# Performance work log

Measured on AMD Instinct MI355X. Metric: run time of the kernel, lower is better.

Reference implementation:

```python
import jax, jax.numpy as jnp
import numpy as np

N = 8192   # nodes
F = 128    # features
ORDER = 4  # polynomial taps


def setup_inputs() -> dict:
    key = jax.random.key(0)
    k1, k2, k3 = jax.random.split(key, 3)
    X = jax.random.normal(k1, (N, F), dtype=jnp.float32)
    # scale GSO so powers don't blow up (spectral-norm-ish normalization)
    S = jax.random.normal(k2, (N, N), dtype=jnp.float32) / jnp.sqrt(jnp.float32(N))
    coefficients = jax.random.uniform(k3, (ORDER,), dtype=jnp.float32)
    return {"X": X, "S": S, "coefficients": coefficients}


def reference(X, S, coefficients):
    # y = sum_{k=0}^{K-1} h_k * S^k X
    Z = X
    y = coefficients[0] * Z
    for k in range(1, ORDER):  # small fixed tap count; loop over taps, not data
        Z = S @ Z              # S^k X, [N, F]
        y = y + coefficients[k] * Z
    return y
```

## Files before the change

kernel.cpp:

```cpp
#include <hip/hip_runtime.h>
#include <hip/hip_bf16.h>
#include <stdint.h>


typedef __attribute__((ext_vector_type(8))) short     bf16x8;
typedef __attribute__((ext_vector_type(8))) uint16_t  u16x8;
typedef __attribute__((ext_vector_type(4))) float     f32x4;

#define NN 8192
#define NF 128
#define ZSTRIDE (8192 + 64)

#define WAITV(n) asm volatile("s_waitcnt vmcnt(" #n ")" ::: "memory")
#define WAITL0   asm volatile("s_waitcnt lgkmcnt(0)" ::: "memory")

__device__ inline uint16_t f2bf(float f) {
    uint32_t u = __builtin_bit_cast(uint32_t, f);
    u += 0x7fffu + ((u >> 16) & 1u);
    return (uint16_t)(u >> 16);
}

__device__ inline void gl2lds16(const void* g, uint8_t* l) {
    __builtin_amdgcn_global_load_lds(
        (const __attribute__((address_space(1))) uint32_t*)g,
        (__attribute__((address_space(3))) uint32_t*)l,
        16, 0, 0);
}

__device__ inline bf16x8 ld16(const uint8_t* p) {
    return __builtin_bit_cast(bf16x8, *(const u16x8*)p);
}

__global__ __launch_bounds__(256) void k_convert(const float* __restrict__ S,
                                                 uint16_t* __restrict__ S16) {
    const size_t n8 = (size_t)NN * NN / 8;
    const size_t stride = (size_t)gridDim.x * 256;
    for (size_t i = (size_t)blockIdx.x * 256 + threadIdx.x; i < n8; i += stride) {
        f32x4 a = __builtin_nontemporal_load((const f32x4*)(S + i * 8));
        f32x4 b = __builtin_nontemporal_load((const f32x4*)(S + i * 8 + 4));
        u16x8 p;
#pragma unroll
        for (int j = 0; j < 4; ++j) { p[j] = f2bf(a[j]); p[j + 4] = f2bf(b[j]); }
        *(u16x8*)(S16 + i * 8) = p;
    }
}

__global__ __launch_bounds__(256) void k_prep(const float* __restrict__ X,
                                              const float* __restrict__ coeff,
                                              float* __restrict__ y,
                                              uint16_t* __restrict__ ZT0) {
    __shared__ float tile[16][NF + 4];
    const int t  = threadIdx.x;
    const int r0 = blockIdx.x * 16;
    const float h0 = coeff[0];
#pragma unroll
    for (int i = 0; i < 2; ++i) {
        int o   = (i * 256 + t) * 4;
        int row = o >> 7, col = o & 127;
        f32x4 v = *(const f32x4*)(X + (size_t)(r0 + row) * NF + col);
        *(f32x4*)&tile[row][col] = v;
        *(f32x4*)(y + (size_t)(r0 + row) * NF + col) = v * h0;
    }
    __syncthreads();
    const int c = t >> 1, rh = t & 1;
    u16x8 pk;
#pragma unroll
    for (int e = 0; e < 8; ++e) pk[e] = f2bf(tile[rh * 8 + e][c]);
    *(u16x8*)(ZT0 + (size_t)c * ZSTRIDE + r0 + rh * 8) = pk;
}

template<int KS>
__global__ __launch_bounds__(512, 4) void k_gemm_bf(
    const uint16_t* __restrict__ S16, const uint16_t* __restrict__ ZTin,
    float* __restrict__ P)
{
    __shared__ __align__(16) uint8_t smem[3][24576];
    const int t = threadIdx.x, lane = t & 63;
    const int w = t >> 6, m = lane & 15, g = lane >> 4;
    const int rt = w & 3, ch = w >> 2;
    const int mt = blockIdx.x & 127, ks = blockIdx.x >> 7;
    const int r0 = mt * 64;
    const int kb = ks * (NN / KS);
    constexpr int NT = (NN / KS) / 64;

    const int srow = t >> 3, sc = t & 7;
    const int scs  = (sc ^ (srow & 7)) << 3;
    const uint16_t* asrc = S16  + (size_t)(r0 + srow) * NN + kb + scs;
    const uint16_t* bsrc = ZTin + (size_t)srow * ZSTRIDE   + kb + scs;

    const int sw   = m & 7;
    const int aoff = (rt * 16 + m) * 128 + ((g ^ sw) << 4);
    const int bof  = 8192 + (ch * 64 + m) * 128 + ((g ^ sw) << 4);

    f32x4 acc[4] = {};

    auto stage = [&](int buf, int kt) {
        const int ko = kt * 64;
        uint8_t* b = smem[buf];
        gl2lds16(asrc + ko, b + t * 16);
        gl2lds16(bsrc + ko, b + 8192 + t * 16);
        gl2lds16(bsrc + (size_t)64 * ZSTRIDE + ko, b + 16384 + t * 16);
    };

    stage(0, 0);
    stage(1, 1);
    int cur = 0;
#pragma unroll 1
    for (int kt = 0; kt < NT; ++kt) {
        if (kt + 2 < NT) {
            int nxt = cur + 2; if (nxt >= 3) nxt -= 3;
            stage(nxt, kt + 2);
            WAITV(6);
        } else if (kt + 2 == NT) {
            WAITV(3);
        } else {
            WAITV(0);
        }
        __builtin_amdgcn_s_barrier();
        __builtin_amdgcn_sched_barrier(0);
        const uint8_t* bb = smem[cur];
        bf16x8 a0 = ld16(bb + aoff);
        bf16x8 a1 = ld16(bb + (aoff ^ 64));
#pragma unroll
        for (int ct = 0; ct < 4; ++ct) {
            acc[ct] = __builtin_amdgcn_mfma_f32_16x16x32_bf16(
                a0, ld16(bb + bof + ct * 16 * 128), acc[ct], 0, 0, 0);
            acc[ct] = __builtin_amdgcn_mfma_f32_16x16x32_bf16(
                a1, ld16(bb + ((bof + ct * 16 * 128) ^ 64)), acc[ct], 0, 0, 0);
        }
        WAITL0;
        __builtin_amdgcn_sched_barrier(0);
        __builtin_amdgcn_s_barrier();
        cur = (cur + 1 == 3) ? 0 : cur + 1;
    }

    float* pb = P + ((size_t)ks * NN + r0 + rt * 16 + 4 * g) * NF + ch * 64 + m;
#pragma unroll
    for (int ct = 0; ct < 4; ++ct)
#pragma unroll
        for (int i = 0; i < 4; ++i)
            pb[(size_t)i * NF + ct * 16] = acc[ct][i];
}

template<int KS, bool WRITE_ZT>
__global__ __launch_bounds__(256) void k_combine(const float* __restrict__ P,
                                                 float* __restrict__ y,
                                                 uint16_t* __restrict__ ZTout,
                                                 const float* __restrict__ coeff,
                                                 int pass) {
    __shared__ float tile[16][NF + 4];
    const int t = threadIdx.x, r0 = blockIdx.x * 16;
    const float hk = coeff[pass];
    const int row = t >> 4, col = (t & 15) * 8;
    const size_t off = (size_t)(r0 + row) * NF + col;
    f32x4 s0 = *(const f32x4*)(P + off);
    f32x4 s1 = *(const f32x4*)(P + off + 4);
#pragma unroll
    for (int k = 1; k < KS; ++k) {
        s0 += *(const f32x4*)(P + (size_t)k * NN * NF + off);
        s1 += *(const f32x4*)(P + (size_t)k * NN * NF + off + 4);
    }
    float* yp = y + off;
    f32x4 y0 = *(const f32x4*)yp, y1 = *(const f32x4*)(yp + 4);
    *(f32x4*)yp       = y0 + hk * s0;
    *(f32x4*)(yp + 4) = y1 + hk * s1;
    if (WRITE_ZT) {
        *(f32x4*)&tile[row][col]     = s0;
        *(f32x4*)&tile[row][col + 4] = s1;
        __syncthreads();
        const int c = t >> 1, rh = t & 1;
        u16x8 pk;
#pragma unroll
        for (int e = 0; e < 8; ++e) pk[e] = f2bf(tile[rh * 8 + e][c]);
        *(u16x8*)(ZTout + (size_t)c * ZSTRIDE + r0 + rh * 8) = pk;
    }
}

template<int KS>
static void run(const float* X, const float* S, const float* coeff, float* y,
                uint16_t* ZT0, uint16_t* ZT1, uint16_t* S16, float* P,
                hipStream_t stream) {
    k_prep<<<dim3(512), dim3(256), 0, stream>>>(X, coeff, y, ZT0);
    k_convert<<<dim3(2048), dim3(256), 0, stream>>>(S, S16);
    k_gemm_bf<KS><<<dim3(128 * KS), dim3(512), 0, stream>>>(S16, ZT0, P);
    k_combine<KS, true ><<<dim3(512), dim3(256), 0, stream>>>(P, y, ZT1, coeff, 1);
    k_gemm_bf<KS><<<dim3(128 * KS), dim3(512), 0, stream>>>(S16, ZT1, P);
    k_combine<KS, true ><<<dim3(512), dim3(256), 0, stream>>>(P, y, ZT0, coeff, 2);
    k_gemm_bf<KS><<<dim3(128 * KS), dim3(512), 0, stream>>>(S16, ZT0, P);
    k_combine<KS, false><<<dim3(512), dim3(256), 0, stream>>>(P, y, nullptr, coeff, 3);
}

extern "C" void kernel_launch(void* const* d_in, const int* in_sizes, int n_in,
                              void* d_out, int out_size, void* d_ws, size_t ws_size,
                              hipStream_t stream) {
    const float* X     = (const float*)d_in[0];
    const float* S     = (const float*)d_in[1];
    const float* coeff = (const float*)d_in[2];
    float* y = (float*)d_out;

    uint8_t* ws = (uint8_t*)d_ws;
    const size_t zb     = ((size_t)NF * ZSTRIDE * sizeof(uint16_t) + 255) & ~(size_t)255;
    const size_t s16b   = (size_t)NN * NN * sizeof(uint16_t);
    const size_t base   = 2 * zb + s16b;
    const size_t pslice = (size_t)NN * NF * sizeof(float);
    uint16_t* ZT0 = (uint16_t*)ws;
    uint16_t* ZT1 = (uint16_t*)(ws + zb);
    uint16_t* S16 = (uint16_t*)(ws + 2 * zb);
    float*    P   = (float*)(ws + base);

    if (ws_size >= base + 4 * pslice)
        run<4>(X, S, coeff, y, ZT0, ZT1, S16, P, stream);
    else if (ws_size >= base + 2 * pslice)
        run<2>(X, S, coeff, y, ZT0, ZT1, S16, P, stream);
    else
        run<1>(X, S, coeff, y, ZT0, ZT1, S16, P, stream);
}
```

Before: 187.0 us.

## Fuse S fp32-to-bf16 conversion into first GEMM and use double buffering

Removes the standalone conversion kernel: each block of the first GEMM converts its own 64-row by K-slice stripe of S to bf16, writes it to the workspace, then runs the GEMM on that stripe, which it reads back from cache. This avoids a separate launch and lets the first GEMM's reads of S16 hit freshly written lines in L2. It also reduces the LDS pipeline from three buffers to two, lowering LDS use per block at the cost of shallower prefetch for all three GEMMs. Each block's conversion is serialized before its GEMM, so there is no overlap inside a block.

```diff
diff --git a/kernel.cpp b/kernel.cpp
--- a/kernel.cpp
+++ b/kernel.cpp
@@ -29,20 +29,6 @@
 
 __device__ inline bf16x8 ld16(const uint8_t* p) {
     return __builtin_bit_cast(bf16x8, *(const u16x8*)p);
-}
-
-__global__ __launch_bounds__(256) void k_convert(const float* __restrict__ S,
-                                                 uint16_t* __restrict__ S16) {
-    const size_t n8 = (size_t)NN * NN / 8;
-    const size_t stride = (size_t)gridDim.x * 256;
-    for (size_t i = (size_t)blockIdx.x * 256 + threadIdx.x; i < n8; i += stride) {
-        f32x4 a = __builtin_nontemporal_load((const f32x4*)(S + i * 8));
-        f32x4 b = __builtin_nontemporal_load((const f32x4*)(S + i * 8 + 4));
-        u16x8 p;
-#pragma unroll
-        for (int j = 0; j < 4; ++j) { p[j] = f2bf(a[j]); p[j + 4] = f2bf(b[j]); }
-        *(u16x8*)(S16 + i * 8) = p;
-    }
 }
 
 __global__ __launch_bounds__(256) void k_prep(const float* __restrict__ X,
@@ -69,56 +55,30 @@
     *(u16x8*)(ZT0 + (size_t)c * ZSTRIDE + r0 + rh * 8) = pk;
 }
 
-template<int KS>
-__global__ __launch_bounds__(512, 4) void k_gemm_bf(
-    const uint16_t* __restrict__ S16, const uint16_t* __restrict__ ZTin,
-    float* __restrict__ P)
-{
-    __shared__ __align__(16) uint8_t smem[3][24576];
-    const int t = threadIdx.x, lane = t & 63;
-    const int w = t >> 6, m = lane & 15, g = lane >> 4;
-    const int rt = w & 3, ch = w >> 2;
-    const int mt = blockIdx.x & 127, ks = blockIdx.x >> 7;
-    const int r0 = mt * 64;
-    const int kb = ks * (NN / KS);
-    constexpr int NT = (NN / KS) / 64;
-
-    const int srow = t >> 3, sc = t & 7;
-    const int scs  = (sc ^ (srow & 7)) << 3;
-    const uint16_t* asrc = S16  + (size_t)(r0 + srow) * NN + kb + scs;
-    const uint16_t* bsrc = ZTin + (size_t)srow * ZSTRIDE   + kb + scs;
-
-    const int sw   = m & 7;
-    const int aoff = (rt * 16 + m) * 128 + ((g ^ sw) << 4);
-    const int bof  = 8192 + (ch * 64 + m) * 128 + ((g ^ sw) << 4);
-
-    f32x4 acc[4] = {};
-
+template<int NT>
+__device__ inline void gemm_core(const uint16_t* asrc, const uint16_t* bsrc,
+                                 uint8_t* smem, int t, f32x4 (&acc)[4],
+                                 int aoff, int bof) {
     auto stage = [&](int buf, int kt) {
         const int ko = kt * 64;
-        uint8_t* b = smem[buf];
+        uint8_t* b = smem + buf * 24576;
         gl2lds16(asrc + ko, b + t * 16);
         gl2lds16(bsrc + ko, b + 8192 + t * 16);
         gl2lds16(bsrc + (size_t)64 * ZSTRIDE + ko, b + 16384 + t * 16);
     };
-
     stage(0, 0);
-    stage(1, 1);
     int cur = 0;
 #pragma unroll 1
     for (int kt = 0; kt < NT; ++kt) {
-        if (kt + 2 < NT) {
-            int nxt = cur + 2; if (nxt >= 3) nxt -= 3;
-            stage(nxt, kt + 2);
-            WAITV(6);
-        } else if (kt + 2 == NT) {
+        if (kt + 1 < NT) {
+            stage(cur ^ 1, kt + 1);
             WAITV(3);
         } else {
             WAITV(0);
         }
         __builtin_amdgcn_s_barrier();
         __builtin_amdgcn_sched_barrier(0);
-        const uint8_t* bb = smem[cur];
+        const uint8_t* bb = smem + cur * 24576;
         bf16x8 a0 = ld16(bb + aoff);
         bf16x8 a1 = ld16(bb + (aoff ^ 64));
 #pragma unroll
@@ -131,8 +91,88 @@
         WAITL0;
         __builtin_amdgcn_sched_barrier(0);
         __builtin_amdgcn_s_barrier();
-        cur = (cur + 1 == 3) ? 0 : cur + 1;
-    }
+        cur ^= 1;
+    }
+}
+
+template<int KS>
+__global__ __launch_bounds__(512, 4) void k_gemm_bf(
+    const uint16_t* __restrict__ S16, const uint16_t* __restrict__ ZTin,
+    float* __restrict__ P)
+{
+    __shared__ __align__(16) uint8_t smem[2][24576];
+    const int t = threadIdx.x, lane = t & 63;
+    const int w = t >> 6, m = lane & 15, g = lane >> 4;
+    const int rt = w & 3, ch = w >> 2;
+    const int mt = blockIdx.x & 127, ks = blockIdx.x >> 7;
+    const int r0 = mt * 64;
+    const int kb = ks * (NN / KS);
+    constexpr int NT = (NN / KS) / 64;
+
+    const int srow = t >> 3, sc = t & 7;
+    const int scs  = (sc ^ (srow & 7)) << 3;
+    const uint16_t* asrc = S16  + (size_t)(r0 + srow) * NN + kb + scs;
+    const uint16_t* bsrc = ZTin + (size_t)srow * ZSTRIDE   + kb + scs;
+
+    const int sw   = m & 7;
+    const int aoff = (rt * 16 + m) * 128 + ((g ^ sw) << 4);
+    const int bof  = 8192 + (ch * 64 + m) * 128 + ((g ^ sw) << 4);
+
+    f32x4 acc[4] = {};
+    gemm_core<NT>(asrc, bsrc, &smem[0][0], t, acc, aoff, bof);
+
+    float* pb = P + ((size_t)ks * NN + r0 + rt * 16 + 4 * g) * NF + ch * 64 + m;
+#pragma unroll
+    for (int ct = 0; ct < 4; ++ct)
+#pragma unroll
+        for (int i = 0; i < 4; ++i)
+            pb[(size_t)i * NF + ct * 16] = acc[ct][i];
+}
+
+template<int KS>
+__global__ __launch_bounds__(512, 4) void k_gemm_cv2(
+    const float* __restrict__ Sf, const uint16_t* __restrict__ S16,
+    const uint16_t* __restrict__ ZTin, float* __restrict__ P)
+{
+    __shared__ __align__(16) uint8_t smem[2][24576];
+    const int t = threadIdx.x, lane = t & 63;
+    const int w = t >> 6, m = lane & 15, g = lane >> 4;
+    const int rt = w & 3, ch = w >> 2;
+    const int mt = blockIdx.x & 127, ks = blockIdx.x >> 7;
+    const int r0 = mt * 64;
+    const int kb = ks * (NN / KS);
+    constexpr int KSL = NN / KS;
+    constexpr int NT  = KSL / 64;
+    constexpr int C8  = KSL / 8;
+    constexpr int ITERS = 64 * KSL / (512 * 8);
+
+    uint16_t* S16w = (uint16_t*)S16;
+#pragma unroll 4
+    for (int it = 0; it < ITERS; ++it) {
+        int id  = it * 512 + t;
+        int row = id / C8, c8 = id % C8;
+        size_t off = (size_t)(r0 + row) * NN + kb + c8 * 8;
+        f32x4 a = *(const f32x4*)(Sf + off);
+        f32x4 b = *(const f32x4*)(Sf + off + 4);
+        u16x8 p;
+#pragma unroll
+        for (int j = 0; j < 4; ++j) { p[j] = f2bf(a[j]); p[j + 4] = f2bf(b[j]); }
+        *(u16x8*)(S16w + off) = p;
+    }
+    WAITV(0);
+    __syncthreads();
+
+    const int srow = t >> 3, sc = t & 7;
+    const int scs  = (sc ^ (srow & 7)) << 3;
+    const uint16_t* asrc = S16  + (size_t)(r0 + srow) * NN + kb + scs;
+    const uint16_t* bsrc = ZTin + (size_t)srow * ZSTRIDE   + kb + scs;
+
+    const int sw   = m & 7;
+    const int aoff = (rt * 16 + m) * 128 + ((g ^ sw) << 4);
+    const int bof  = 8192 + (ch * 64 + m) * 128 + ((g ^ sw) << 4);
+
+    f32x4 acc[4] = {};
+    gemm_core<NT>(asrc, bsrc, &smem[0][0], t, acc, aoff, bof);
 
     float* pb = P + ((size_t)ks * NN + r0 + rt * 16 + 4 * g) * NF + ch * 64 + m;
 #pragma unroll
@@ -181,8 +221,7 @@
                 uint16_t* ZT0, uint16_t* ZT1, uint16_t* S16, float* P,
                 hipStream_t stream) {
     k_prep<<<dim3(512), dim3(256), 0, stream>>>(X, coeff, y, ZT0);
-    k_convert<<<dim3(2048), dim3(256), 0, stream>>>(S, S16);
-    k_gemm_bf<KS><<<dim3(128 * KS), dim3(512), 0, stream>>>(S16, ZT0, P);
+    k_gemm_cv2<KS><<<dim3(128 * KS), dim3(512), 0, stream>>>(S, S16, ZT0, P);
     k_combine<KS, true ><<<dim3(512), dim3(256), 0, stream>>>(P, y, ZT1, coeff, 1);
     k_gemm_bf<KS><<<dim3(128 * KS), dim3(512), 0, stream>>>(S16, ZT1, P);
     k_combine<KS, true ><<<dim3(512), dim3(256), 0, stream>>>(P, y, ZT0, coeff, 2);
```

Result: slower. 196.1 us (+4.8%).

## Pre-tile S into contiguous bf16 blocks per GEMM workgroup tile

Applied to the files above, without the earlier changes.

The fp32-to-bf16 conversion of S now writes it in a tiled layout, so each GEMM workgroup's A operand for every k-step is one contiguous 8 KB block instead of 64 strided row segments. This makes the global-to-LDS loads in the three GEMM passes fully sequential, aiming to improve DRAM/cache efficiency. The split-K factor is hardcoded to 4, so the fallback paths for smaller workspaces are gone. The conversion kernel now uses normal rather than nontemporal loads plus an LDS staging step.

```diff
diff --git a/kernel.cpp b/kernel.cpp
--- a/kernel.cpp
+++ b/kernel.cpp
@@ -29,20 +29,6 @@
 
 __device__ inline bf16x8 ld16(const uint8_t* p) {
     return __builtin_bit_cast(bf16x8, *(const u16x8*)p);
-}
-
-__global__ __launch_bounds__(256) void k_convert(const float* __restrict__ S,
-                                                 uint16_t* __restrict__ S16) {
-    const size_t n8 = (size_t)NN * NN / 8;
-    const size_t stride = (size_t)gridDim.x * 256;
-    for (size_t i = (size_t)blockIdx.x * 256 + threadIdx.x; i < n8; i += stride) {
-        f32x4 a = __builtin_nontemporal_load((const f32x4*)(S + i * 8));
-        f32x4 b = __builtin_nontemporal_load((const f32x4*)(S + i * 8 + 4));
-        u16x8 p;
-#pragma unroll
-        for (int j = 0; j < 4; ++j) { p[j] = f2bf(a[j]); p[j + 4] = f2bf(b[j]); }
-        *(u16x8*)(S16 + i * 8) = p;
-    }
 }
 
 __global__ __launch_bounds__(256) void k_prep(const float* __restrict__ X,
@@ -69,9 +55,41 @@
     *(u16x8*)(ZT0 + (size_t)c * ZSTRIDE + r0 + rh * 8) = pk;
 }
 
-template<int KS>
+__global__ __launch_bounds__(256) void k_convert_t(const float* __restrict__ S,
+                                                   uint16_t* __restrict__ S16T) {
+    __shared__ __align__(16) uint16_t lds[16384];
+    const int t = threadIdx.x, bx = blockIdx.x;
+    const int mt = bx & 127, ks = bx >> 7;
+    const int r0 = mt * 64, kb = ks * 2048;
+    uint16_t* tb = S16T + (size_t)(mt * 4 + ks) * 131072;
+
+#pragma unroll 1
+    for (int kc = 0; kc < 8; ++kc) {
+#pragma unroll
+        for (int si = 0; si < 8; ++si) {
+            int id = si * 256 + t;
+            int rr = id >> 5, c8 = id & 31;
+            const float* src = S + (size_t)(r0 + rr) * NN + kb + kc * 256 + c8 * 8;
+            f32x4 a = *(const f32x4*)src;
+            f32x4 b = *(const f32x4*)(src + 4);
+            u16x8 p;
+#pragma unroll
+            for (int j = 0; j < 4; ++j) { p[j] = f2bf(a[j]); p[j + 4] = f2bf(b[j]); }
+            *(u16x8*)&lds[((c8 >> 3) * 64 + rr) * 64 + (c8 & 7) * 8] = p;
+        }
+        __syncthreads();
+        uint16_t* dst = tb + kc * 16384;
+#pragma unroll
+        for (int si = 0; si < 8; ++si) {
+            int id = si * 256 + t;
+            *(u16x8*)(dst + id * 8) = *(const u16x8*)&lds[id * 8];
+        }
+        __syncthreads();
+    }
+}
+
 __global__ __launch_bounds__(512, 4) void k_gemm_bf(
-    const uint16_t* __restrict__ S16, const uint16_t* __restrict__ ZTin,
+    const uint16_t* __restrict__ S16T, const uint16_t* __restrict__ ZTin,
     float* __restrict__ P)
 {
     __shared__ __align__(16) uint8_t smem[3][24576];
@@ -80,13 +98,14 @@
     const int rt = w & 3, ch = w >> 2;
     const int mt = blockIdx.x & 127, ks = blockIdx.x >> 7;
     const int r0 = mt * 64;
-    const int kb = ks * (NN / KS);
-    constexpr int NT = (NN / KS) / 64;
+    const int kb = ks * 2048;
+    constexpr int NT = 32;
 
     const int srow = t >> 3, sc = t & 7;
-    const int scs  = (sc ^ (srow & 7)) << 3;
-    const uint16_t* asrc = S16  + (size_t)(r0 + srow) * NN + kb + scs;
-    const uint16_t* bsrc = ZTin + (size_t)srow * ZSTRIDE   + kb + scs;
+    const uint16_t* asrc = S16T + (size_t)(mt * 4 + ks) * 131072
+                           + srow * 64 + ((sc ^ (srow & 7)) << 3);
+    const uint16_t* bsrc = ZTin + (size_t)srow * ZSTRIDE + kb
+                           + ((sc ^ (srow & 7)) << 3);
 
     const int sw   = m & 7;
     const int aoff = (rt * 16 + m) * 128 + ((g ^ sw) << 4);
@@ -95,11 +114,10 @@
     f32x4 acc[4] = {};
 
     auto stage = [&](int buf, int kt) {
-        const int ko = kt * 64;
         uint8_t* b = smem[buf];
-        gl2lds16(asrc + ko, b + t * 16);
-        gl2lds16(bsrc + ko, b + 8192 + t * 16);
-        gl2lds16(bsrc + (size_t)64 * ZSTRIDE + ko, b + 16384 + t * 16);
+        gl2lds16(asrc + kt * 4096, b + t * 16);
+        gl2lds16(bsrc + kt * 64, b + 8192 + t * 16);
+        gl2lds16(bsrc + (size_t)64 * ZSTRIDE + kt * 64, b + 16384 + t * 16);
     };
 
     stage(0, 0);
@@ -142,7 +160,7 @@
             pb[(size_t)i * NF + ct * 16] = acc[ct][i];
 }
 
-template<int KS, bool WRITE_ZT>
+template<bool WRITE_ZT>
 __global__ __launch_bounds__(256) void k_combine(const float* __restrict__ P,
                                                  float* __restrict__ y,
                                                  uint16_t* __restrict__ ZTout,
@@ -156,7 +174,7 @@
     f32x4 s0 = *(const f32x4*)(P + off);
     f32x4 s1 = *(const f32x4*)(P + off + 4);
 #pragma unroll
-    for (int k = 1; k < KS; ++k) {
+    for (int k = 1; k < 4; ++k) {
         s0 += *(const f32x4*)(P + (size_t)k * NN * NF + off);
         s1 += *(const f32x4*)(P + (size_t)k * NN * NF + off + 4);
     }
@@ -176,20 +194,6 @@
     }
 }
 
-template<int KS>
-static void run(const float* X, const float* S, const float* coeff, float* y,
-                uint16_t* ZT0, uint16_t* ZT1, uint16_t* S16, float* P,
-                hipStream_t stream) {
-    k_prep<<<dim3(512), dim3(256), 0, stream>>>(X, coeff, y, ZT0);
-    k_convert<<<dim3(2048), dim3(256), 0, stream>>>(S, S16);
-    k_gemm_bf<KS><<<dim3(128 * KS), dim3(512), 0, stream>>>(S16, ZT0, P);
-    k_combine<KS, true ><<<dim3(512), dim3(256), 0, stream>>>(P, y, ZT1, coeff, 1);
-    k_gemm_bf<KS><<<dim3(128 * KS), dim3(512), 0, stream>>>(S16, ZT1, P);
-    k_combine<KS, true ><<<dim3(512), dim3(256), 0, stream>>>(P, y, ZT0, coeff, 2);
-    k_gemm_bf<KS><<<dim3(128 * KS), dim3(512), 0, stream>>>(S16, ZT0, P);
-    k_combine<KS, false><<<dim3(512), dim3(256), 0, stream>>>(P, y, nullptr, coeff, 3);
-}
-
 extern "C" void kernel_launch(void* const* d_in, const int* in_sizes, int n_in,
                               void* d_out, int out_size, void* d_ws, size_t ws_size,
                               hipStream_t stream) {
@@ -208,10 +212,12 @@
     uint16_t* S16 = (uint16_t*)(ws + 2 * zb);
     float*    P   = (float*)(ws + base);
 
-    if (ws_size >= base + 4 * pslice)
-        run<4>(X, S, coeff, y, ZT0, ZT1, S16, P, stream);
-    else if (ws_size >= base + 2 * pslice)
-        run<2>(X, S, coeff, y, ZT0, ZT1, S16, P, stream);
-    else
-        run<1>(X, S, coeff, y, ZT0, ZT1, S16, P, stream);
-}
+    k_prep<<<dim3(512), dim3(256), 0, stream>>>(X, coeff, y, ZT0);
+    k_convert_t<<<dim3(512), dim3(256), 0, stream>>>(S, S16);
+    k_gemm_bf<<<dim3(512), dim3(512), 0, stream>>>(S16, ZT0, P);
+    k_combine<true ><<<dim3(512), dim3(256), 0, stream>>>(P, y, ZT1, coeff, 1);
+    k_gemm_bf<<<dim3(512), dim3(512), 0, stream>>>(S16, ZT1, P);
+    k_combine<true ><<<dim3(512), dim3(256), 0, stream>>>(P, y, ZT0, coeff, 2);
+    k_gemm_bf<<<dim3(512), dim3(512), 0, stream>>>(S16, ZT0, P);
+    k_combine<false><<<dim3(512), dim3(256), 0, stream>>>(P, y, nullptr, coeff, 3);
+}
```

New measurement: 212.7 us. 1.14x slower.
